# Optimization experiments

Measured on AMD Instinct MI355X. Metric: run time of the kernel, lower is better.

Reference implementation:

```python
import jax, jax.numpy as jnp
import numpy as np

N_NODES = 100000


def gcn_conv(x, src, dst, ew, W, b, n_nodes):
    """PyG-style GCNConv: add self-loops, symmetric degree normalization,
    linear transform, scatter-add aggregation, bias."""
    loop = jnp.arange(n_nodes)
    src_f = jnp.concatenate([src, loop])          # [E+N]
    dst_f = jnp.concatenate([dst, loop])          # [E+N]
    ew_f = jnp.concatenate([ew, jnp.ones((n_nodes,), dtype=ew.dtype)])
    deg = jax.ops.segment_sum(ew_f, dst_f, num_segments=n_nodes)  # [N]
    dinv = jnp.where(deg > 0, jax.lax.rsqrt(deg), 0.0)
    norm = dinv[src_f] * ew_f * dinv[dst_f]       # [E+N]
    h = x @ W.T                                   # [N, out]
    msg = h[src_f] * norm[:, None]                # [E+N, out] gather + scale
    out = jax.ops.segment_sum(msg, dst_f, num_segments=n_nodes)
    return out + b


def prelu(x, a):
    return jnp.where(x >= 0, x, a * x)


def setup_inputs() -> dict:
    key = jax.random.key(0)
    k = jax.random.split(key, 8)
    in_c, out_c = 256, 128
    n_edges = 1600000
    x = jax.random.normal(k[0], (N_NODES, in_c), dtype=jnp.float32)
    edge_index = jax.random.randint(k[1], (2, n_edges), 0, N_NODES, dtype=jnp.int64)
    edge_weight = jax.random.uniform(k[2], (n_edges,), dtype=jnp.float32)
    W1 = jax.random.normal(k[3], (out_c, in_c), dtype=jnp.float32) / np.sqrt(in_c)
    b1 = jnp.zeros((out_c,), dtype=jnp.float32)
    W2 = jax.random.normal(k[4], (out_c, out_c), dtype=jnp.float32) / np.sqrt(out_c)
    b2 = jnp.zeros((out_c,), dtype=jnp.float32)
    a = jnp.asarray(0.25, dtype=jnp.float32)  # PReLU single shared parameter
    return {"x": x, "edge_index": edge_index, "edge_weight": edge_weight,
            "W1": W1, "b1": b1, "W2": W2, "b2": b2, "a": a}


def reference(x, edge_index, edge_weight, W1, b1, W2, b2, a):
    src, dst = edge_index[0], edge_index[1]
    h1 = prelu(gcn_conv(x, src, dst, edge_weight, W1, b1, N_NODES), a)
    h2 = prelu(gcn_conv(h1, src, dst, edge_weight, W2, b2, N_NODES), a)
    return (h1, h2)
```

## Files before the change

kernel.cpp:

```cpp
#include <hip/hip_runtime.h>


static __device__ __forceinline__ float4 ld4(const float* p) { return *(const float4*)p; }

static __device__ __forceinline__ unsigned short f2bf(float f) {
    unsigned u = __float_as_uint(f);
    u += 0x7fff + ((u >> 16) & 1);
    return (unsigned short)(u >> 16);
}
static __device__ __forceinline__ float bf2f(unsigned short h) {
    return __uint_as_float(((unsigned)h) << 16);
}

typedef __attribute__((ext_vector_type(8))) short short8v;
typedef __attribute__((ext_vector_type(4))) float f32x4;

static __device__ __forceinline__ int eidx(const void* ei, int flag, long long idx) {
    if (flag) return (int)((const long long*)ei)[idx];
    return ((const int*)ei)[idx];
}

#define CNT_SH 24
#define DEG_SCALE 262144.0f
#define DEG_INV   3.814697265625e-06f
#define Q15_INV   3.0517578125e-05f

__global__ void k_detect(const int* ei, int* flag) {
    __shared__ int anynz;
    if (threadIdx.x == 0) anynz = 0;
    __syncthreads();
    if (ei[2 * threadIdx.x + 1] != 0) anynz = 1;
    __syncthreads();
    if (threadIdx.x == 0) *flag = (anynz == 0) ? 1 : 0;
}

static __device__ __forceinline__ void packW_body(const float* __restrict__ W,
                                                  unsigned short* __restrict__ Bp,
                                                  int t, int kbits) {
    int K = 1 << kbits;
    int col = t >> kbits, k = t & (K - 1);
    int nt = col >> 4, ks = k >> 5;
    int lane = (col & 15) | (((k >> 3) & 3) << 4);
    int j = k & 7;
    Bp[((((size_t)nt * (K >> 5) + ks) * 64 + lane) << 3) + j] = f2bf(W[t]);
}

__global__ __launch_bounds__(256) void k_prep(unsigned* __restrict__ packed, int N,
                                              const float* __restrict__ W1,
                                              unsigned short* __restrict__ bp1,
                                              const float* __restrict__ W2,
                                              unsigned short* __restrict__ bp2,
                                              int nbInit) {
    int b = blockIdx.x;
    if (b < nbInit) {
        int i = b * 256 + threadIdx.x;
        if (i < N) packed[i] = 0u;
    } else if (b < nbInit + 128) {
        int t = (b - nbInit) * 256 + threadIdx.x;
        packW_body(W1, bp1, t, 8);
    } else {
        int t = (b - nbInit - 128) * 256 + threadIdx.x;
        packW_body(W2, bp2, t, 7);
    }
}

static __device__ __forceinline__ void count_body(const void* __restrict__ ei,
                                                  const float* __restrict__ ew,
                                                  int flag,
                                                  unsigned* __restrict__ packed,
                                                  unsigned char* __restrict__ rank,
                                                  int E, int cbid) {
    int base = cbid * 2048 + threadIdx.x;
    int d[8]; unsigned inc[8]; bool ok[8];
    #pragma unroll
    for (int u = 0; u < 8; ++u) {
        int e = base + u * 256;
        ok[u] = e < E;
        if (ok[u]) {
            d[u] = eidx(ei, flag, (long long)E + e);
            inc[u] = (1u << CNT_SH) | (unsigned)(ew[e] * DEG_SCALE);
        }
    }
    unsigned old[8];
    #pragma unroll
    for (int u = 0; u < 8; ++u)
        if (ok[u]) old[u] = atomicAdd(&packed[d[u]], inc[u]);
    #pragma unroll
    for (int u = 0; u < 8; ++u)
        if (ok[u]) rank[base + u * 256] = (unsigned char)(old[u] >> CNT_SH);
}

template <int K>
static __device__ __forceinline__ void gemm_body(const float* __restrict__ X,
                                                 const unsigned short* __restrict__ Bp,
                                                 unsigned short* __restrict__ Hb,
                                                 int M, int gbid) {
    constexpr int KS = K / 32;
    int wave = threadIdx.x >> 6, lane = threadIdx.x & 63;
    int row0 = gbid * 128 + wave * 32;
    int r0 = row0 + (lane & 15);      if (r0 >= M) r0 = M - 1;
    int r1 = row0 + 16 + (lane & 15); if (r1 >= M) r1 = M - 1;
    int kc = (lane >> 4) * 8;
    const float* x0 = X + (size_t)r0 * K + kc;
    const float* x1 = X + (size_t)r1 * K + kc;

    f32x4 acc[2][8] = {};
    #pragma unroll 2
    for (int ks = 0; ks < KS; ++ks) {
        float4 a0 = ld4(x0 + ks * 32), a1 = ld4(x0 + ks * 32 + 4);
        float4 c0 = ld4(x1 + ks * 32), c1 = ld4(x1 + ks * 32 + 4);
        short8v af0, af1;
        af0[0] = (short)f2bf(a0.x); af0[1] = (short)f2bf(a0.y);
        af0[2] = (short)f2bf(a0.z); af0[3] = (short)f2bf(a0.w);
        af0[4] = (short)f2bf(a1.x); af0[5] = (short)f2bf(a1.y);
        af0[6] = (short)f2bf(a1.z); af0[7] = (short)f2bf(a1.w);
        af1[0] = (short)f2bf(c0.x); af1[1] = (short)f2bf(c0.y);
        af1[2] = (short)f2bf(c0.z); af1[3] = (short)f2bf(c0.w);
        af1[4] = (short)f2bf(c1.x); af1[5] = (short)f2bf(c1.y);
        af1[6] = (short)f2bf(c1.z); af1[7] = (short)f2bf(c1.w);
        #pragma unroll
        for (int nt = 0; nt < 8; ++nt) {
            short8v bf = *(const short8v*)&Bp[(((size_t)nt * KS + ks) * 64 + lane) * 8];
            acc[0][nt] = __builtin_amdgcn_mfma_f32_16x16x32_bf16(af0, bf, acc[0][nt], 0, 0, 0);
            acc[1][nt] = __builtin_amdgcn_mfma_f32_16x16x32_bf16(af1, bf, acc[1][nt], 0, 0, 0);
        }
    }
    #pragma unroll
    for (int rg = 0; rg < 2; ++rg) {
        int orow0 = row0 + rg * 16 + (lane >> 4) * 4;
        #pragma unroll
        for (int nt = 0; nt < 8; ++nt) {
            int col = nt * 16 + (lane & 15);
            #pragma unroll
            for (int j = 0; j < 4; ++j) {
                int r = orow0 + j;
                if (r < M) Hb[(size_t)r * 128 + col] = f2bf(acc[rg][nt][j]);
            }
        }
    }
}

__global__ __launch_bounds__(256) void k_count_gemm1(
        const void* __restrict__ ei, const float* __restrict__ ew,
        const int* __restrict__ flagp, unsigned* __restrict__ packed,
        unsigned char* __restrict__ rank, int E,
        const float* __restrict__ X, const unsigned short* __restrict__ Bp,
        unsigned short* __restrict__ Hb, int M,
        int nbCount, int nbGemm, int cgrps, int ggrps) {
    int grp = blockIdx.x >> 3, ln = blockIdx.x & 7;
    int tot = cgrps + ggrps;
    int cb = (int)(((long long)grp * cgrps) / tot);
    int ca = (int)(((long long)(grp + 1) * cgrps) / tot);
    if (ca > cb) {
        int id = cb * 8 + ln;
        if (id < nbCount) count_body(ei, ew, *flagp, packed, rank, E, id);
    } else {
        int id = (grp - cb) * 8 + ln;
        if (id < nbGemm) gemm_body<256>(X, Bp, Hb, M, id);
    }
}

__global__ __launch_bounds__(256) void k_gemm2(const float* __restrict__ X,
                                               const unsigned short* __restrict__ Bp,
                                               unsigned short* __restrict__ Hb, int M) {
    gemm_body<128>(X, Bp, Hb, M, blockIdx.x);
}

__global__ __launch_bounds__(256) void k_blocksum(const unsigned* packed,
                                                  int* bsum, int N) {
    int i = blockIdx.x * 256 + threadIdx.x;
    int v = i < N ? (int)(packed[i] >> CNT_SH) : 0;
    for (int d = 32; d > 0; d >>= 1) v += __shfl_down(v, d, 64);
    __shared__ int wsum[4];
    int lane = threadIdx.x & 63, wid = threadIdx.x >> 6;
    if (lane == 0) wsum[wid] = v;
    __syncthreads();
    if (threadIdx.x == 0) bsum[blockIdx.x] = wsum[0] + wsum[1] + wsum[2] + wsum[3];
}

__global__ __launch_bounds__(512) void k_scan_bsum(int* bsum, int nb) {
    int t = threadIdx.x;
    int v = (t < nb) ? bsum[t] : 0;
    int orig = v;
    int lane = t & 63, wid = t >> 6;
    for (int d = 1; d < 64; d <<= 1) { int n = __shfl_up(v, d, 64); if (lane >= d) v += n; }
    __shared__ int wsum[8];
    if (lane == 63) wsum[wid] = v;
    __syncthreads();
    int woff = 0;
    for (int w = 0; w < 8; ++w) if (w < wid) woff += wsum[w];
    if (t < nb) bsum[t] = v - orig + woff;
}

__global__ __launch_bounds__(256) void k_scan_final(const unsigned* packed,
                                                    const int* bsum,
                                                    int* offs, float* dinv,
                                                    int N, int E) {
    int b = blockIdx.x, t = threadIdx.x;
    int i = b * 256 + t;
    unsigned pk = (i < N) ? packed[i] : 0u;
    int v = (int)(pk >> CNT_SH);
    int orig = v;
    int lane = t & 63, wid = t >> 6;
    for (int d = 1; d < 64; d <<= 1) { int n = __shfl_up(v, d, 64); if (lane >= d) v += n; }
    __shared__ int wsum[4];
    if (lane == 63) wsum[wid] = v;
    __syncthreads();
    int woff = bsum[b];
    for (int w = 0; w < 4; ++w) if (w < wid) woff += wsum[w];
    if (i < N) {
        offs[i] = v - orig + woff;
        float dg = 1.0f + (float)(pk & 0xFFFFFFu) * DEG_INV;
        dinv[i] = rsqrtf(dg);
    }
    if (i == 0) offs[N] = E;
}

__global__ __launch_bounds__(256) void k_scatter(const void* __restrict__ ei,
                                                 const float* __restrict__ ew,
                                                 const int* __restrict__ flagp,
                                                 const float* __restrict__ dinv,
                                                 const int* __restrict__ offs,
                                                 const unsigned char* __restrict__ rank,
                                                 unsigned* __restrict__ spair, int E) {
    const int flag = *flagp;
    int e = blockIdx.x * 256 + threadIdx.x;
    if (e < E) {
        int s = eidx(ei, flag, e);
        int d = eidx(ei, flag, (long long)E + e);
        int p = offs[d] + (int)rank[e];
        float nrm = dinv[s] * ew[e] * dinv[d];
        unsigned q = (unsigned)(nrm * 32768.0f + 0.5f);
        spair[p] = ((unsigned)s << 15) | q;
    }
}

__global__ __launch_bounds__(256) void k_agg(const unsigned short* __restrict__ Hb,
                                             const int* __restrict__ offs,
                                             const unsigned* __restrict__ spair,
                                             const float* __restrict__ dinv,
                                             const float* __restrict__ bias,
                                             const float* __restrict__ a_ptr,
                                             float* __restrict__ Out, int N) {
    int g = blockIdx.x * 8 + (threadIdx.x >> 5);
    int lane = threadIdx.x & 31;
    if (g >= N) return;
    float alpha = a_ptr[0];
    float di = dinv[g];
    float4 acc = ld4(bias + lane * 4);
    ushort4 hv = *(const ushort4*)(Hb + (size_t)g * 128 + lane * 4);
    float sw = di * di;
    acc.x += bf2f(hv.x) * sw; acc.y += bf2f(hv.y) * sw;
    acc.z += bf2f(hv.z) * sw; acc.w += bf2f(hv.w) * sw;
    int j0 = offs[g], j1 = offs[g + 1];
    for (int jb = j0; jb < j1; jb += 32) {
        int j = jb + lane;
        unsigned sp = 0u;
        if (j < j1) sp = spair[j];
        int cnt = j1 - jb; if (cnt > 32) cnt = 32;
        int full = cnt & ~3, i = 0;
        for (; i < full; i += 4) {
            unsigned p0 = __shfl(sp, i,     32), p1 = __shfl(sp, i + 1, 32);
            unsigned p2 = __shfl(sp, i + 2, 32), p3 = __shfl(sp, i + 3, 32);
            int   s0 = p0 >> 15, s1 = p1 >> 15, s2 = p2 >> 15, s3 = p3 >> 15;
            float w0 = (float)(p0 & 0x7FFFu) * Q15_INV;
            float w1 = (float)(p1 & 0x7FFFu) * Q15_INV;
            float w2 = (float)(p2 & 0x7FFFu) * Q15_INV;
            float w3 = (float)(p3 & 0x7FFFu) * Q15_INV;
            ushort4 h0 = *(const ushort4*)(Hb + (size_t)s0 * 128 + lane * 4);
            ushort4 h1 = *(const ushort4*)(Hb + (size_t)s1 * 128 + lane * 4);
            ushort4 h2 = *(const ushort4*)(Hb + (size_t)s2 * 128 + lane * 4);
            ushort4 h3 = *(const ushort4*)(Hb + (size_t)s3 * 128 + lane * 4);
            acc.x += bf2f(h0.x) * w0; acc.y += bf2f(h0.y) * w0;
            acc.z += bf2f(h0.z) * w0; acc.w += bf2f(h0.w) * w0;
            acc.x += bf2f(h1.x) * w1; acc.y += bf2f(h1.y) * w1;
            acc.z += bf2f(h1.z) * w1; acc.w += bf2f(h1.w) * w1;
            acc.x += bf2f(h2.x) * w2; acc.y += bf2f(h2.y) * w2;
            acc.z += bf2f(h2.z) * w2; acc.w += bf2f(h2.w) * w2;
            acc.x += bf2f(h3.x) * w3; acc.y += bf2f(h3.y) * w3;
            acc.z += bf2f(h3.z) * w3; acc.w += bf2f(h3.w) * w3;
        }
        for (; i < cnt; ++i) {
            unsigned pv = __shfl(sp, i, 32);
            int   sv = pv >> 15;
            float wv = (float)(pv & 0x7FFFu) * Q15_INV;
            ushort4 h4 = *(const ushort4*)(Hb + (size_t)sv * 128 + lane * 4);
            acc.x += bf2f(h4.x) * wv; acc.y += bf2f(h4.y) * wv;
            acc.z += bf2f(h4.z) * wv; acc.w += bf2f(h4.w) * wv;
        }
    }
    acc.x = acc.x >= 0.f ? acc.x : alpha * acc.x;
    acc.y = acc.y >= 0.f ? acc.y : alpha * acc.y;
    acc.z = acc.z >= 0.f ? acc.z : alpha * acc.z;
    acc.w = acc.w >= 0.f ? acc.w : alpha * acc.w;
    *(float4*)(Out + (size_t)g * 128 + lane * 4) = acc;
}

extern "C" void kernel_launch(void* const* d_in, const int* in_sizes, int n_in,
                              void* d_out, int out_size, void* d_ws, size_t ws_size,
                              hipStream_t stream) {
    const float* x  = (const float*)d_in[0];
    const void*  ei = d_in[1];
    const float* ew = (const float*)d_in[2];
    const float* W1 = (const float*)d_in[3];
    const float* b1 = (const float*)d_in[4];
    const float* W2 = (const float*)d_in[5];
    const float* b2 = (const float*)d_in[6];
    const float* ap = (const float*)d_in[7];
    const int N = in_sizes[0] / 256;
    const int E = in_sizes[2];

    float* out1 = (float*)d_out;
    float* out2 = out1 + (size_t)N * 128;

    char* p = (char*)d_ws;
    auto alloc = [&](size_t bytes) { void* r = (void*)p; p += (bytes + 255) & ~(size_t)255; return r; };
    unsigned* packed = (unsigned*)alloc((size_t)N * 4);
    float* dinv  = (float*)alloc((size_t)N * 4);
    int*   offs  = (int*)  alloc((size_t)(N + 1) * 4);
    int*   bsum  = (int*)  alloc((size_t)((N + 255) / 256) * 4);
    int*   flag  = (int*)  alloc(256);
    unsigned char* rank = (unsigned char*)alloc((size_t)E);
    unsigned* spair = (unsigned*)alloc((size_t)E * 4);
    unsigned short* hb  = (unsigned short*)alloc((size_t)N * 128 * 2);
    unsigned short* bp1 = (unsigned short*)alloc((size_t)128 * 256 * 2);
    unsigned short* bp2 = (unsigned short*)alloc((size_t)128 * 128 * 2);

    const int nbN    = (N + 255) / 256;
    const int nbE    = (E + 255) / 256;
    const int nbCnt  = (E + 2047) / 2048;
    const int nbGemm = (N + 127) / 128;
    const int cgrps  = (nbCnt + 7) / 8;
    const int ggrps  = (nbGemm + 7) / 8;

    k_detect<<<1, 256, 0, stream>>>((const int*)ei, flag);
    k_prep<<<nbN + 128 + 64, 256, 0, stream>>>(packed, N, W1, bp1, W2, bp2, nbN);
    k_count_gemm1<<<(cgrps + ggrps) * 8, 256, 0, stream>>>(
        ei, ew, flag, packed, rank, E, x, bp1, hb, N, nbCnt, nbGemm, cgrps, ggrps);
    k_blocksum<<<nbN, 256, 0, stream>>>(packed, bsum, N);
    k_scan_bsum<<<1, 512, 0, stream>>>(bsum, nbN);
    k_scan_final<<<nbN, 256, 0, stream>>>(packed, bsum, offs, dinv, N, E);
    k_scatter<<<nbE, 256, 0, stream>>>(ei, ew, flag, dinv, offs, rank, spair, E);

    k_agg<<<(N + 7) / 8, 256, 0, stream>>>(hb, offs, spair, dinv, b1, ap, out1, N);
    k_gemm2<<<nbGemm, 256, 0, stream>>>(out1, bp2, hb, N);
    k_agg<<<(N + 7) / 8, 256, 0, stream>>>(hb, offs, spair, dinv, b2, ap, out2, N);
}
```

Baseline: 270.9 us.

## Fuse layer-1 aggregation with layer-2 GEMM and fold flag detection into prep

The first aggregation kernel now keeps each block's 64 aggregated rows in LDS as bf16 and runs the 128x128 second-layer MFMA GEMM directly on them, writing H2 to a new buffer. This removes the separate gemm2 launch and its re-read of out1 from global memory. The edge-index format detection moves into an extra block of the prep kernel, saving one launch. In exchange, aggregation blocks now hold 16KB of LDS and use 64 nodes per block, which may lower occupancy and leave tail imbalance on the latency-bound gather.

```diff
diff --git a/kernel.cpp b/kernel.cpp
--- a/kernel.cpp
+++ b/kernel.cpp
@@ -24,15 +24,6 @@
 #define DEG_SCALE 262144.0f
 #define DEG_INV   3.814697265625e-06f
 #define Q15_INV   3.0517578125e-05f
-
-__global__ void k_detect(const int* ei, int* flag) {
-    __shared__ int anynz;
-    if (threadIdx.x == 0) anynz = 0;
-    __syncthreads();
-    if (ei[2 * threadIdx.x + 1] != 0) anynz = 1;
-    __syncthreads();
-    if (threadIdx.x == 0) *flag = (anynz == 0) ? 1 : 0;
-}
 
 static __device__ __forceinline__ void packW_body(const float* __restrict__ W,
                                                   unsigned short* __restrict__ Bp,
@@ -50,6 +41,8 @@
                                               unsigned short* __restrict__ bp1,
                                               const float* __restrict__ W2,
                                               unsigned short* __restrict__ bp2,
+                                              const int* __restrict__ ei_raw,
+                                              int* __restrict__ flag,
                                               int nbInit) {
     int b = blockIdx.x;
     if (b < nbInit) {
@@ -58,9 +51,16 @@
     } else if (b < nbInit + 128) {
         int t = (b - nbInit) * 256 + threadIdx.x;
         packW_body(W1, bp1, t, 8);
-    } else {
+    } else if (b < nbInit + 192) {
         int t = (b - nbInit - 128) * 256 + threadIdx.x;
         packW_body(W2, bp2, t, 7);
+    } else {
+        __shared__ int anynz;
+        if (threadIdx.x == 0) anynz = 0;
+        __syncthreads();
+        if (ei_raw[2 * threadIdx.x + 1] != 0) anynz = 1;
+        __syncthreads();
+        if (threadIdx.x == 0) *flag = (anynz == 0) ? 1 : 0;
     }
 }
 
@@ -158,12 +158,6 @@
         int id = (grp - cb) * 8 + ln;
         if (id < nbGemm) gemm_body<256>(X, Bp, Hb, M, id);
     }
-}
-
-__global__ __launch_bounds__(256) void k_gemm2(const float* __restrict__ X,
-                                               const unsigned short* __restrict__ Bp,
-                                               unsigned short* __restrict__ Hb, int M) {
-    gemm_body<128>(X, Bp, Hb, M, blockIdx.x);
 }
 
 __global__ __launch_bounds__(256) void k_blocksum(const unsigned* packed,
@@ -235,19 +229,14 @@
     }
 }
 
-__global__ __launch_bounds__(256) void k_agg(const unsigned short* __restrict__ Hb,
-                                             const int* __restrict__ offs,
-                                             const unsigned* __restrict__ spair,
-                                             const float* __restrict__ dinv,
-                                             const float* __restrict__ bias,
-                                             const float* __restrict__ a_ptr,
-                                             float* __restrict__ Out, int N) {
-    int g = blockIdx.x * 8 + (threadIdx.x >> 5);
-    int lane = threadIdx.x & 31;
-    if (g >= N) return;
-    float alpha = a_ptr[0];
+static __device__ __forceinline__ float4 agg_node(const unsigned short* __restrict__ Hb,
+                                                  const int* __restrict__ offs,
+                                                  const unsigned* __restrict__ spair,
+                                                  const float* __restrict__ dinv,
+                                                  float4 bv, float alpha,
+                                                  int g, int lane) {
     float di = dinv[g];
-    float4 acc = ld4(bias + lane * 4);
+    float4 acc = bv;
     ushort4 hv = *(const ushort4*)(Hb + (size_t)g * 128 + lane * 4);
     float sw = di * di;
     acc.x += bf2f(hv.x) * sw; acc.y += bf2f(hv.y) * sw;
@@ -293,6 +282,82 @@
     acc.y = acc.y >= 0.f ? acc.y : alpha * acc.y;
     acc.z = acc.z >= 0.f ? acc.z : alpha * acc.z;
     acc.w = acc.w >= 0.f ? acc.w : alpha * acc.w;
+    return acc;
+}
+
+__global__ __launch_bounds__(256) void k_agg_gemm(
+        const unsigned short* __restrict__ Hb,
+        const int* __restrict__ offs,
+        const unsigned* __restrict__ spair,
+        const float* __restrict__ dinv,
+        const float* __restrict__ bias,
+        const float* __restrict__ a_ptr,
+        const unsigned short* __restrict__ Bp2,
+        float* __restrict__ Out1,
+        unsigned short* __restrict__ Hb2, int N) {
+    __shared__ unsigned short rows[64 * 128];
+    int grp = threadIdx.x >> 5, lane5 = threadIdx.x & 31;
+    int base = blockIdx.x * 64;
+    float alpha = a_ptr[0];
+    float4 bv = ld4(bias + lane5 * 4);
+    #pragma unroll 2
+    for (int t = 0; t < 8; ++t) {
+        int lrow = t * 8 + grp;
+        int g = base + lrow;
+        float4 acc;
+        if (g < N) {
+            acc = agg_node(Hb, offs, spair, dinv, bv, alpha, g, lane5);
+            *(float4*)(Out1 + (size_t)g * 128 + lane5 * 4) = acc;
+        } else {
+            acc.x = acc.y = acc.z = acc.w = 0.f;
+        }
+        int sel = (lane5 * 4) ^ ((lrow & 7) << 3);
+        ushort4 rb;
+        rb.x = f2bf(acc.x); rb.y = f2bf(acc.y);
+        rb.z = f2bf(acc.z); rb.w = f2bf(acc.w);
+        *(ushort4*)&rows[lrow * 128 + sel] = rb;
+    }
+    __syncthreads();
+    int wave = threadIdx.x >> 6, lane = threadIdx.x & 63;
+    int rbase = wave * 16;
+    f32x4 acc2[8] = {};
+    #pragma unroll
+    for (int ks = 0; ks < 4; ++ks) {
+        int arow = rbase + (lane & 15);
+        int koff = ks * 32 + (lane >> 4) * 8;
+        int sidx = koff ^ ((arow & 7) << 3);
+        short8v af = *(const short8v*)&rows[arow * 128 + sidx];
+        #pragma unroll
+        for (int nt = 0; nt < 8; ++nt) {
+            short8v bf = *(const short8v*)&Bp2[(((size_t)nt * 4 + ks) * 64 + lane) * 8];
+            acc2[nt] = __builtin_amdgcn_mfma_f32_16x16x32_bf16(af, bf, acc2[nt], 0, 0, 0);
+        }
+    }
+    int orow0 = base + rbase + (lane >> 4) * 4;
+    #pragma unroll
+    for (int nt = 0; nt < 8; ++nt) {
+        int col = nt * 16 + (lane & 15);
+        #pragma unroll
+        for (int j = 0; j < 4; ++j) {
+            int r = orow0 + j;
+            if (r < N) Hb2[(size_t)r * 128 + col] = f2bf(acc2[nt][j]);
+        }
+    }
+}
+
+__global__ __launch_bounds__(256) void k_agg(const unsigned short* __restrict__ Hb,
+                                             const int* __restrict__ offs,
+                                             const unsigned* __restrict__ spair,
+                                             const float* __restrict__ dinv,
+                                             const float* __restrict__ bias,
+                                             const float* __restrict__ a_ptr,
+                                             float* __restrict__ Out, int N) {
+    int g = blockIdx.x * 8 + (threadIdx.x >> 5);
+    int lane = threadIdx.x & 31;
+    if (g >= N) return;
+    float alpha = a_ptr[0];
+    float4 bv = ld4(bias + lane * 4);
+    float4 acc = agg_node(Hb, offs, spair, dinv, bv, alpha, g, lane);
     *(float4*)(Out + (size_t)g * 128 + lane * 4) = acc;
 }
 
@@ -323,6 +388,7 @@
     unsigned char* rank = (unsigned char*)alloc((size_t)E);
     unsigned* spair = (unsigned*)alloc((size_t)E * 4);
     unsigned short* hb  = (unsigned short*)alloc((size_t)N * 128 * 2);
+    unsigned short* hb2 = (unsigned short*)alloc((size_t)N * 128 * 2);
     unsigned short* bp1 = (unsigned short*)alloc((size_t)128 * 256 * 2);
     unsigned short* bp2 = (unsigned short*)alloc((size_t)128 * 128 * 2);
 
@@ -333,8 +399,8 @@
     const int cgrps  = (nbCnt + 7) / 8;
     const int ggrps  = (nbGemm + 7) / 8;
 
-    k_detect<<<1, 256, 0, stream>>>((const int*)ei, flag);
-    k_prep<<<nbN + 128 + 64, 256, 0, stream>>>(packed, N, W1, bp1, W2, bp2, nbN);
+    k_prep<<<nbN + 128 + 64 + 1, 256, 0, stream>>>(packed, N, W1, bp1, W2, bp2,
+                                                   (const int*)ei, flag, nbN);
     k_count_gemm1<<<(cgrps + ggrps) * 8, 256, 0, stream>>>(
         ei, ew, flag, packed, rank, E, x, bp1, hb, N, nbCnt, nbGemm, cgrps, ggrps);
     k_blocksum<<<nbN, 256, 0, stream>>>(packed, bsum, N);
@@ -342,7 +408,7 @@
     k_scan_final<<<nbN, 256, 0, stream>>>(packed, bsum, offs, dinv, N, E);
     k_scatter<<<nbE, 256, 0, stream>>>(ei, ew, flag, dinv, offs, rank, spair, E);
 
-    k_agg<<<(N + 7) / 8, 256, 0, stream>>>(hb, offs, spair, dinv, b1, ap, out1, N);
-    k_gemm2<<<nbGemm, 256, 0, stream>>>(out1, bp2, hb, N);
-    k_agg<<<(N + 7) / 8, 256, 0, stream>>>(hb, offs, spair, dinv, b2, ap, out2, N);
-}
+    k_agg_gemm<<<(N + 63) / 64, 256, 0, stream>>>(hb, offs, spair, dinv, b1, ap,
+                                                  bp2, out1, hb2, N);
+    k_agg<<<(N + 7) / 8, 256, 0, stream>>>(hb2, offs, spair, dinv, b2, ap, out2, N);
+}
```

Result: slower. 291.5 us (+7.6%).
